# Performance work log

Hardware: AMD Instinct MI355X
Metric: run time of the kernel (lower is better)

## Reference

```python
import jax, jax.numpy as jnp
import numpy as np

EMBED_DIM = 1024
NUM_HEADS = 16
HEAD_DIM = EMBED_DIM // NUM_HEADS
SCALING = (1.0 / HEAD_DIM) ** 0.5


def setup_inputs() -> dict:
    key = jax.random.key(0)
    ks = jax.random.split(key, 9)
    d = EMBED_DIM
    return {
        "hidden_states": jax.random.normal(ks[0], (4, 2048, d), dtype=jnp.float32),
        "q_w": jax.random.normal(ks[1], (d, d), dtype=jnp.float32) * 0.02,
        "q_b": jax.random.normal(ks[2], (d,), dtype=jnp.float32) * 0.02,
        "k_w": jax.random.normal(ks[3], (d, d), dtype=jnp.float32) * 0.02,
        "k_b": jax.random.normal(ks[4], (d,), dtype=jnp.float32) * 0.02,
        "v_w": jax.random.normal(ks[5], (d, d), dtype=jnp.float32) * 0.02,
        "v_b": jax.random.normal(ks[6], (d,), dtype=jnp.float32) * 0.02,
        "out_w": jax.random.normal(ks[7], (d, d), dtype=jnp.float32) * 0.02,
        "out_b": jax.random.normal(ks[8], (d,), dtype=jnp.float32) * 0.02,
    }


def _shape(x, bsz, seq, nh, hd):
    # [B, T, E] -> [B, H, T, Hd]
    return x.reshape(bsz, seq, nh, hd).transpose(0, 2, 1, 3)


def reference(hidden_states, q_w, q_b, k_w, k_b, v_w, v_b, out_w, out_b):
    bsz, tgt_len, _ = hidden_states.shape
    # torch Linear: y = x @ W.T + b; query scaled by sqrt(1/head_dim)
    q = (hidden_states @ q_w.T + q_b) * SCALING
    k = hidden_states @ k_w.T + k_b
    v = hidden_states @ v_w.T + v_b
    q = _shape(q, bsz, tgt_len, NUM_HEADS, HEAD_DIM)
    k = _shape(k, bsz, tgt_len, NUM_HEADS, HEAD_DIM)
    v = _shape(v, bsz, tgt_len, NUM_HEADS, HEAD_DIM)
    # [B, H, T, S]
    attn_weights = jnp.einsum("bhtd,bhsd->bhts", q, k)
    attn_weights = jax.nn.softmax(attn_weights, axis=-1)
    # [B, H, T, Hd] -> [B, T, E]
    attn_output = jnp.einsum("bhts,bhsd->bhtd", attn_weights, v)
    attn_output = attn_output.transpose(0, 2, 1, 3).reshape(bsz, tgt_len, EMBED_DIM)
    return attn_output @ out_w.T + out_b
```

## Files before the change

### kernel.cpp

```cpp
#include <hip/hip_runtime.h>
#include <hip/hip_bf16.h>
#include <cstdint>
#include <math.h>

typedef uint16_t u16;
typedef __attribute__((ext_vector_type(8))) short short8;
typedef __attribute__((ext_vector_type(2))) float floatx2;
typedef __attribute__((ext_vector_type(4))) float floatx4;
typedef __attribute__((ext_vector_type(16))) float floatx16;

__device__ __forceinline__ float bf2f(u16 u) {
  return __uint_as_float(((uint32_t)u) << 16);
}
__device__ __forceinline__ u16 f2bf(float f) {
  uint32_t u = __float_as_uint(f);
  u += 0x7FFF + ((u >> 16) & 1);
  return (u16)(u >> 16);
}

#if __has_builtin(__builtin_amdgcn_exp2f)
#define EXP2(x) __builtin_amdgcn_exp2f(x)
#else
#define EXP2(x) exp2f(x)
#endif

__device__ __forceinline__ void glds16(const void* g, void* l) {
  __builtin_amdgcn_global_load_lds(
      (const __attribute__((address_space(1))) void*)g,
      (__attribute__((address_space(3))) void*)l, 16, 0, 0);
}

__device__ __forceinline__ bool detect_fp32(const u16* __restrict__ hs) {
  int big = 0;
#pragma unroll
  for (int i = 0; i < 128; ++i) {
    const int e = (hs[i] >> 7) & 0xFF;
    big += (e >= 140);
  }
  return big > 0;
}

__device__ __forceinline__ void conv_blk(
    const void* __restrict__ src, u16* __restrict__ dst, int i, bool f32)
{
  if (f32) {
    const float4 v = ((const float4*)src)[i];
    ushort4 d;
    d.x = f2bf(v.x); d.y = f2bf(v.y); d.z = f2bf(v.z); d.w = f2bf(v.w);
    ((ushort4*)dst)[i] = d;
  } else {
    ((ushort4*)dst)[i] = ((const ushort4*)src)[i];
  }
}

__global__ __launch_bounds__(256) void convert_all(
    const void* __restrict__ hs, const void* __restrict__ qw,
    const void* __restrict__ kw, const void* __restrict__ vw,
    const void* __restrict__ ow, const void* __restrict__ qb,
    const void* __restrict__ kb, const void* __restrict__ vb,
    const void* __restrict__ ob,
    u16* __restrict__ d_hs, u16* __restrict__ d_qw, u16* __restrict__ d_kw,
    u16* __restrict__ d_vw, u16* __restrict__ d_ow, u16* __restrict__ d_qb,
    u16* __restrict__ d_kb, u16* __restrict__ d_vb, u16* __restrict__ d_ob)
{
  const bool f32 = detect_fp32((const u16*)hs);
  const int bid = blockIdx.x;
  const int tid = threadIdx.x;
  if (bid < 2048) {
#pragma unroll
    for (int k = 0; k < 4; ++k)
      conv_blk(hs, d_hs, bid * 1024 + k * 256 + tid, f32);
  } else if (bid < 2048 + 1024) {
    const int w = (bid - 2048) >> 8;
    const int base = ((bid - 2048) & 255) * 1024;
    const void* s = (w == 0) ? qw : (w == 1) ? kw : (w == 2) ? vw : ow;
    u16* d        = (w == 0) ? d_qw : (w == 1) ? d_kw : (w == 2) ? d_vw : d_ow;
#pragma unroll
    for (int k = 0; k < 4; ++k)
      conv_blk(s, d, base + k * 256 + tid, f32);
  } else {
    const int w = bid - 3072;
    const void* s = (w == 0) ? qb : (w == 1) ? kb : (w == 2) ? vb : ob;
    u16* d        = (w == 0) ? d_qb : (w == 1) ? d_kb : (w == 2) ? d_vb : d_ob;
    conv_blk(s, d, tid, f32);
  }
}

template <int MODE>
__device__ __forceinline__ void gemm_body(
    const u16* __restrict__ A, const u16* __restrict__ W,
    const u16* __restrict__ bias, void* __restrict__ vout,
    float scale, u16* As, u16* Bs, int bx, int by, bool f32out)
{
  constexpr int KD = 1024;
  const int tid  = threadIdx.x;
  const int lane = tid & 63;
  const int l15  = lane & 15;
  const int quad = lane >> 4;
  const int wid  = tid >> 6;
  const int bm = by * 128, bn = bx * 128;
  const int wm = (wid >> 1) * 64, wn = (wid & 1) * 64;

  floatx4 acc[4][4];
#pragma unroll
  for (int i = 0; i < 4; ++i)
#pragma unroll
    for (int j = 0; j < 4; ++j)
#pragma unroll
      for (int r = 0; r < 4; ++r) acc[i][j][r] = 0.0f;

  const int c0 = tid, c1 = tid + 256;
  const u16* Ag0 = A + (size_t)(bm + (c0 >> 2)) * KD + (c0 & 3) * 8;
  const u16* Ag1 = A + (size_t)(bm + (c1 >> 2)) * KD + (c1 & 3) * 8;
  const u16* Wg0 = W + (size_t)(bn + (c0 >> 2)) * KD + (c0 & 3) * 8;
  const u16* Wg1 = W + (size_t)(bn + (c1 >> 2)) * KD + (c1 & 3) * 8;
  u16* As0 = As + c0 * 8;  u16* As1 = As + c1 * 8;
  u16* Bs0 = Bs + c0 * 8;  u16* Bs1 = Bs + c1 * 8;

  for (int kt = 0; kt < KD / 64; ++kt) {
    const int ko = kt * 64;
    glds16(Ag0 + ko, As0);
    glds16(Ag1 + ko, As1);
    glds16(Wg0 + ko, Bs0);
    glds16(Wg1 + ko, Bs1);
    glds16(Ag0 + ko + 32, As0 + 4096);
    glds16(Ag1 + ko + 32, As1 + 4096);
    glds16(Wg0 + ko + 32, Bs0 + 4096);
    glds16(Wg1 + ko + 32, Bs1 + 4096);
    __syncthreads();
#pragma unroll
    for (int h = 0; h < 2; ++h) {
      const u16* Ah = As + h * 4096;
      const u16* Bh = Bs + h * 4096;
      short8 af[4], bf[4];
#pragma unroll
      for (int mb = 0; mb < 4; ++mb)
        af[mb] = *(const short8*)&Ah[(wm + mb * 16 + l15) * 32 + quad * 8];
#pragma unroll
      for (int nb = 0; nb < 4; ++nb)
        bf[nb] = *(const short8*)&Bh[(wn + nb * 16 + l15) * 32 + quad * 8];
#pragma unroll
      for (int mb = 0; mb < 4; ++mb)
#pragma unroll
        for (int nb = 0; nb < 4; ++nb) {
          if (MODE == 2)
            acc[mb][nb] = __builtin_amdgcn_mfma_f32_16x16x32_bf16(
                bf[nb], af[mb], acc[mb][nb], 0, 0, 0);
          else
            acc[mb][nb] = __builtin_amdgcn_mfma_f32_16x16x32_bf16(
                af[mb], bf[nb], acc[mb][nb], 0, 0, 0);
        }
    }
    __syncthreads();
  }

  if (MODE == 2) {
#pragma unroll
    for (int nb = 0; nb < 4; ++nb)
#pragma unroll
      for (int r = 0; r < 4; ++r) {
        const int wrow = bn + wn + nb * 16 + quad * 4 + r;
        const float bv = bf2f(bias[wrow]);
        const int h = wrow >> 6, d = wrow & 63;
        u16* out = (u16*)vout;
#pragma unroll
        for (int mb = 0; mb < 4; ++mb) {
          const int tcol = bm + wm + mb * 16 + l15;
          const int b = tcol >> 11, t = tcol & 2047;
          out[((size_t)(b * 16 + h) * 64 + d) * 2048 + t] =
              f2bf((acc[mb][nb][r] + bv) * scale);
        }
      }
  } else {
    float bias_v[4];
#pragma unroll
    for (int nb = 0; nb < 4; ++nb) bias_v[nb] = bf2f(bias[bn + wn + nb * 16 + l15]);
#pragma unroll
    for (int mb = 0; mb < 4; ++mb)
#pragma unroll
      for (int nb = 0; nb < 4; ++nb)
#pragma unroll
        for (int r = 0; r < 4; ++r) {
          const int row = bm + wm + mb * 16 + quad * 4 + r;
          const int col = bn + wn + nb * 16 + l15;
          const float v = (acc[mb][nb][r] + bias_v[nb]) * scale;
          if (MODE == 0) {
            if (f32out) ((float*)vout)[(size_t)row * 1024 + col] = v;
            else        ((u16*)vout)[(size_t)row * 1024 + col] = f2bf(v);
          } else {
            const int b = row >> 11, t = row & 2047;
            const int h = col >> 6, d = col & 63;
            ((u16*)vout)[(((size_t)(b * 16 + h)) * 2048 + t) * 64 + d] = f2bf(v);
          }
        }
  }
}

__global__ __launch_bounds__(256, 3) void gemm_qkv(
    const u16* __restrict__ A,
    const u16* __restrict__ Wq, const u16* __restrict__ Wk, const u16* __restrict__ Wv,
    const u16* __restrict__ bq, const u16* __restrict__ bk, const u16* __restrict__ bv,
    u16* __restrict__ Oq, u16* __restrict__ Ok, u16* __restrict__ Ov)
{
  __shared__ u16 As[2 * 128 * 32];
  __shared__ u16 Bs[2 * 128 * 32];
  const int lid = blockIdx.x + 8 * blockIdx.y + 512 * blockIdx.z;
  const int w   = (lid & 7) * 192 + (lid >> 3);
  const int bx  = w & 7;
  const int by  = (w >> 3) & 63;
  const int z   = w >> 9;
  if (z < 2) {
    const u16* Wt   = z ? Wk : Wq;
    const u16* bias = z ? bk : bq;
    u16* out        = z ? Ok : Oq;
    const float scale = z ? 1.0f : 0.125f;
    gemm_body<1>(A, Wt, bias, out, scale, As, Bs, bx, by, false);
  } else {
    gemm_body<2>(A, Wv, bv, Ov, 1.0f, As, Bs, bx, by, false);
  }
}

__global__ __launch_bounds__(256, 3) void gemm_out_proj(
    const u16* __restrict__ A, const u16* __restrict__ W,
    const u16* __restrict__ bias, void* __restrict__ out,
    const u16* __restrict__ probe)
{
  __shared__ u16 As[2 * 128 * 32];
  __shared__ u16 Bs[2 * 128 * 32];
  const bool f32 = detect_fp32(probe);
  const int lid = blockIdx.x + 8 * blockIdx.y;
  const int w   = (lid & 7) * 64 + (lid >> 3);
  const int bx  = w & 7;
  const int by  = w >> 3;
  gemm_body<0>(A, W, bias, out, 1.0f, As, Bs, bx, by, f32);
}

__global__ __launch_bounds__(256, 4) void attn_fused(
    const u16* __restrict__ Q, const u16* __restrict__ K,
    const u16* __restrict__ VT, u16* __restrict__ O)
{
  constexpr int T = 2048, D = 64;
  constexpr int KS = 72;
  __shared__ u16 Ks[128 * KS];
  __shared__ float Linv[128];

  const int tid  = threadIdx.x;
  const int lane = tid & 63;
  const int l31  = lane & 31;
  const int half = lane >> 5;
  const int wid  = tid >> 6;
  const int lid = blockIdx.x + 16 * blockIdx.y;
  const int wkid = (lid & 7) * 128 + (lid >> 3);
  const int qt = wkid & 15;
  const int bh = wkid >> 4;
  const int q0w = wid * 32;

  const u16* Qb = Q + (size_t)bh * T * D + (size_t)qt * 128 * D;
  const u16* Kb = K + (size_t)bh * T * D;
  const u16* Vb = VT + (size_t)bh * D * T;
  const u16* Vl0 = Vb + (size_t)l31 * T + half * 8;
  const u16* Vl1 = Vb + (size_t)(32 + l31) * T + half * 8;

  short8 qf[4];
#pragma unroll
  for (int kk = 0; kk < 4; ++kk)
    qf[kk] = *(const short8*)&Qb[(q0w + l31) * D + kk * 16 + half * 8];

  floatx16 o_acc[2];
#pragma unroll
  for (int dt = 0; dt < 2; ++dt)
#pragma unroll
    for (int i = 0; i < 16; ++i) o_acc[dt][i] = 0.0f;
  floatx2 l01 = {0.0f, 0.0f}, l23 = {0.0f, 0.0f};

  const floatx2 L2E2 = {1.4426950408889634f, 1.4426950408889634f};

#pragma unroll 1
  for (int kt = 0; kt < T / 128; ++kt) {
    const u16* Kt = Kb + (size_t)kt * 128 * D;
#pragma unroll
    for (int j = 0; j < 4; ++j) {
      const int c = tid + j * 256;
      const int r = c >> 3, d0 = (c & 7) * 8;
      *(short8*)&Ks[r * KS + d0] = *(const short8*)&Kt[r * D + d0];
    }
    __syncthreads();

#pragma unroll
    for (int t = 0; t < 4; ++t) {
      floatx16 s;
#pragma unroll
      for (int i = 0; i < 16; ++i) s[i] = 0.0f;
      __builtin_amdgcn_s_setprio(1);
#pragma unroll
      for (int kk = 0; kk < 4; ++kk) {
        const short8 kf = *(const short8*)&Ks[(t * 32 + l31) * KS + kk * 16 + half * 8];
        s = __builtin_amdgcn_mfma_f32_32x32x16_bf16(kf, qf[kk], s, 0, 0, 0);
      }
      __builtin_amdgcn_s_setprio(0);
      uint32_t e[4][2];
#pragma unroll
      for (int g = 0; g < 4; ++g) {
        const floatx2 s01 = {s[4 * g + 0], s[4 * g + 1]};
        const floatx2 s23 = {s[4 * g + 2], s[4 * g + 3]};
        floatx2 t01, t23;
        asm("v_pk_mul_f32 %0, %1, %2" : "=v"(t01) : "v"(s01), "v"(L2E2));
        asm("v_pk_mul_f32 %0, %1, %2" : "=v"(t23) : "v"(s23), "v"(L2E2));
        floatx2 p01, p23;
        p01.x = EXP2(fminf(t01.x, 44.f));
        p01.y = EXP2(fminf(t01.y, 44.f));
        p23.x = EXP2(fminf(t23.x, 44.f));
        p23.y = EXP2(fminf(t23.y, 44.f));
        asm("v_pk_add_f32 %0, %0, %1" : "+v"(l01) : "v"(p01));
        asm("v_pk_add_f32 %0, %0, %1" : "+v"(l23) : "v"(p23));
        asm("v_cvt_pk_bf16_f32 %0, %1, %2" : "=v"(e[g][0]) : "v"(p01.x), "v"(p01.y));
        asm("v_cvt_pk_bf16_f32 %0, %1, %2" : "=v"(e[g][1]) : "v"(p23.x), "v"(p23.y));
      }
#pragma unroll
      for (int c = 0; c < 2; ++c) {
        uint32_t a0 = e[2 * c][0], b0 = e[2 * c + 1][0];
        uint32_t a1 = e[2 * c][1], b1 = e[2 * c + 1][1];
        asm("v_permlane32_swap_b32 %0, %1" : "+v"(a0), "+v"(b0));
        asm("v_permlane32_swap_b32 %0, %1" : "+v"(a1), "+v"(b1));
        union { uint32_t u[4]; short8 v; } pu;
        pu.u[0] = a0; pu.u[1] = a1; pu.u[2] = b0; pu.u[3] = b1;
        const short8 pf = pu.v;
        const int off = kt * 128 + (2 * t + c) * 16;
        const short8 vf0 = *(const short8*)&Vl0[off];
        const short8 vf1 = *(const short8*)&Vl1[off];
        __builtin_amdgcn_s_setprio(1);
        o_acc[0] = __builtin_amdgcn_mfma_f32_32x32x16_bf16(pf, vf0, o_acc[0], 0, 0, 0);
        o_acc[1] = __builtin_amdgcn_mfma_f32_32x32x16_bf16(pf, vf1, o_acc[1], 0, 0, 0);
        __builtin_amdgcn_s_setprio(0);
      }
    }
    __syncthreads();
  }

  const float l_acc = (l01.x + l01.y) + (l23.x + l23.y);
  uint32_t lu0 = __float_as_uint(l_acc), lu1 = lu0;
  asm("v_permlane32_swap_b32 %0, %1" : "+v"(lu0), "+v"(lu1));
  const float l_full = l_acc + __uint_as_float(half ? lu0 : lu1);
  Linv[q0w + l31] = 1.0f / l_full;

  const int b = bh >> 4, h = bh & 15;
  u16* Ob = O + ((size_t)b * 2048 + (size_t)qt * 128) * 1024 + h * 64;
  float invs[16];
#pragma unroll
  for (int i = 0; i < 16; ++i)
    invs[i] = Linv[q0w + (i & 3) + 8 * (i >> 2) + 4 * half];
#pragma unroll
  for (int dt = 0; dt < 2; ++dt)
#pragma unroll
    for (int i = 0; i < 16; ++i) {
      const int qrow = q0w + (i & 3) + 8 * (i >> 2) + 4 * half;
      Ob[(size_t)qrow * 1024 + dt * 32 + l31] = f2bf((float)o_acc[dt][i] * invs[i]);
    }
}

extern "C" void kernel_launch(void* const* d_in, const int* in_sizes, int n_in,
                              void* d_out, int out_size, void* d_ws, size_t ws_size,
                              hipStream_t stream) {
  const u16* hs_probe = (const u16*)d_in[0];

  const size_t TE = (size_t)4 * 2048 * 1024;
  const size_t WE = (size_t)1024 * 1024;
  u16* hsB = (u16*)d_ws;
  u16* Qb  = hsB + TE;
  u16* Kb  = Qb + TE;
  u16* Vb  = Kb + TE;
  u16* Ob  = Vb + TE;
  u16* qwB = Ob + TE;
  u16* kwB = qwB + WE;
  u16* vwB = kwB + WE;
  u16* owB = vwB + WE;
  u16* qbB = owB + WE;
  u16* kbB = qbB + 1024;
  u16* vbB = kbB + 1024;
  u16* obB = vbB + 1024;

  dim3 bb(256);
  convert_all<<<dim3(3076), bb, 0, stream>>>(
      d_in[0], d_in[1], d_in[3], d_in[5], d_in[7],
      d_in[2], d_in[4], d_in[6], d_in[8],
      hsB, qwB, kwB, vwB, owB, qbB, kbB, vbB, obB);

  gemm_qkv<<<dim3(8, 64, 3), bb, 0, stream>>>(
      hsB, qwB, kwB, vwB, qbB, kbB, vbB, Qb, Kb, Vb);
  attn_fused<<<dim3(16, 64), bb, 0, stream>>>(Qb, Kb, Vb, Ob);
  gemm_out_proj<<<dim3(8, 64), bb, 0, stream>>>(Ob, owB, obB, d_out, hs_probe);
}
```

Before: 328.3 us.

## Double-buffer K and V tiles in LDS with register prefetch in attention

The attention kernel now stages both K and the transposed V through double-buffered shared memory in 64-key tiles. The next tile is prefetched into registers while the current tile is being computed, and one barrier per iteration replaces two. V fragments now come from LDS rather than straight from global memory. Launch bounds drop from 4 to 2 blocks per CU, which may lower occupancy but gives the compiler more registers.

Result: faster. 288.0 us (-12.3%).

```diff
diff --git a/kernel.cpp b/kernel.cpp
--- a/kernel.cpp
+++ b/kernel.cpp
@@ -235,13 +235,14 @@
   gemm_body<0>(A, W, bias, out, 1.0f, As, Bs, bx, by, f32);
 }
 
-__global__ __launch_bounds__(256, 4) void attn_fused(
+__global__ __launch_bounds__(256, 2) void attn_fused(
     const u16* __restrict__ Q, const u16* __restrict__ K,
     const u16* __restrict__ VT, u16* __restrict__ O)
 {
   constexpr int T = 2048, D = 64;
   constexpr int KS = 72;
-  __shared__ u16 Ks[128 * KS];
+  __shared__ u16 Ks[2][64 * KS];
+  __shared__ u16 Vts[2][64 * KS];
   __shared__ float Linv[128];
 
   const int tid  = threadIdx.x;
@@ -258,8 +259,9 @@
   const u16* Qb = Q + (size_t)bh * T * D + (size_t)qt * 128 * D;
   const u16* Kb = K + (size_t)bh * T * D;
   const u16* Vb = VT + (size_t)bh * D * T;
-  const u16* Vl0 = Vb + (size_t)l31 * T + half * 8;
-  const u16* Vl1 = Vb + (size_t)(32 + l31) * T + half * 8;
+
+  const int c0r = tid >> 3,        c0o = (tid & 7) * 8;
+  const int c1r = (tid + 256) >> 3, c1o = ((tid + 256) & 7) * 8;
 
   short8 qf[4];
 #pragma unroll
@@ -275,26 +277,38 @@
 
   const floatx2 L2E2 = {1.4426950408889634f, 1.4426950408889634f};
 
+  short8 krg0, krg1, vrg0, vrg1;
+  krg0 = *(const short8*)&Kb[(size_t)c0r * D + c0o];
+  krg1 = *(const short8*)&Kb[(size_t)c1r * D + c1o];
+  vrg0 = *(const short8*)&Vb[(size_t)c0r * T + c0o];
+  vrg1 = *(const short8*)&Vb[(size_t)c1r * T + c1o];
+
 #pragma unroll 1
-  for (int kt = 0; kt < T / 128; ++kt) {
-    const u16* Kt = Kb + (size_t)kt * 128 * D;
-#pragma unroll
-    for (int j = 0; j < 4; ++j) {
-      const int c = tid + j * 256;
-      const int r = c >> 3, d0 = (c & 7) * 8;
-      *(short8*)&Ks[r * KS + d0] = *(const short8*)&Kt[r * D + d0];
+  for (int kt = 0; kt < T / 64; ++kt) {
+    const int cur = kt & 1;
+    *(short8*)&Ks[cur][c0r * KS + c0o] = krg0;
+    *(short8*)&Ks[cur][c1r * KS + c1o] = krg1;
+    *(short8*)&Vts[cur][c0r * KS + c0o] = vrg0;
+    *(short8*)&Vts[cur][c1r * KS + c1o] = vrg1;
+    __syncthreads();
+    if (kt + 1 < T / 64) {
+      const u16* Kt = Kb + (size_t)(kt + 1) * 64 * D;
+      krg0 = *(const short8*)&Kt[(size_t)c0r * D + c0o];
+      krg1 = *(const short8*)&Kt[(size_t)c1r * D + c1o];
+      vrg0 = *(const short8*)&Vb[(size_t)c0r * T + (kt + 1) * 64 + c0o];
+      vrg1 = *(const short8*)&Vb[(size_t)c1r * T + (kt + 1) * 64 + c1o];
     }
-    __syncthreads();
-
-#pragma unroll
-    for (int t = 0; t < 4; ++t) {
+
+#pragma unroll
+    for (int t = 0; t < 2; ++t) {
       floatx16 s;
 #pragma unroll
       for (int i = 0; i < 16; ++i) s[i] = 0.0f;
       __builtin_amdgcn_s_setprio(1);
 #pragma unroll
       for (int kk = 0; kk < 4; ++kk) {
-        const short8 kf = *(const short8*)&Ks[(t * 32 + l31) * KS + kk * 16 + half * 8];
+        const short8 kf =
+            *(const short8*)&Ks[cur][(t * 32 + l31) * KS + kk * 16 + half * 8];
         s = __builtin_amdgcn_mfma_f32_32x32x16_bf16(kf, qf[kk], s, 0, 0, 0);
       }
       __builtin_amdgcn_s_setprio(0);
@@ -325,27 +339,30 @@
         union { uint32_t u[4]; short8 v; } pu;
         pu.u[0] = a0; pu.u[1] = a1; pu.u[2] = b0; pu.u[3] = b1;
         const short8 pf = pu.v;
-        const int off = kt * 128 + (2 * t + c) * 16;
-        const short8 vf0 = *(const short8*)&Vl0[off];
-        const short8 vf1 = *(const short8*)&Vl1[off];
+        const int kkp = 2 * t + c;
+        const short8 vf0 =
+            *(const short8*)&Vts[cur][l31 * KS + kkp * 16 + half * 8];
+        const short8 vf1 =
+            *(const short8*)&Vts[cur][(32 + l31) * KS + kkp * 16 + half * 8];
         __builtin_amdgcn_s_setprio(1);
         o_acc[0] = __builtin_amdgcn_mfma_f32_32x32x16_bf16(pf, vf0, o_acc[0], 0, 0, 0);
         o_acc[1] = __builtin_amdgcn_mfma_f32_32x32x16_bf16(pf, vf1, o_acc[1], 0, 0, 0);
         __builtin_amdgcn_s_setprio(0);
       }
     }
-    __syncthreads();
   }
 
   const float l_acc = (l01.x + l01.y) + (l23.x + l23.y);
   uint32_t lu0 = __float_as_uint(l_acc), lu1 = lu0;
   asm("v_permlane32_swap_b32 %0, %1" : "+v"(lu0), "+v"(lu1));
   const float l_full = l_acc + __uint_as_float(half ? lu0 : lu1);
+  __syncthreads();
   Linv[q0w + l31] = 1.0f / l_full;
 
   const int b = bh >> 4, h = bh & 15;
   u16* Ob = O + ((size_t)b * 2048 + (size_t)qt * 128) * 1024 + h * 64;
   float invs[16];
+  __syncthreads();
 #pragma unroll
   for (int i = 0; i < 16; ++i)
     invs[i] = Linv[q0w + (i & 3) + 8 * (i >> 2) + 4 * half];
```
